# Kernel optimization log

Measured on AMD Instinct MI355X. Metric: run time of the kernel, lower is better.

Reference implementation:

```python
import jax, jax.numpy as jnp
import numpy as np

B = 16        # graphs per batch
NPG = 4096    # nodes per graph
N = B * NPG
EPG = 32768   # edges per graph
E = B * EPG
F_NODE, F_EDGE, G, H, A = 8, 4, 16, 128, 10


def setup_inputs() -> dict:
    key = jax.random.key(0)
    ks = jax.random.split(key, 32)
    x = jax.random.normal(ks[0], (N, F_NODE), jnp.float32)
    # random intra-graph edges, offset into the batched node id space
    src = jax.random.randint(ks[1], (B, EPG), 0, NPG)
    dst = jax.random.randint(ks[2], (B, EPG), 0, NPG)
    off = (jnp.arange(B) * NPG)[:, None]
    edge_index = jnp.stack([(src + off).reshape(-1), (dst + off).reshape(-1)]).astype(jnp.int64)
    edge_attr = jax.random.normal(ks[3], (E, F_EDGE), jnp.float32)
    global_state = jax.random.normal(ks[4], (B, G), jnp.float32)
    current_pipe_nodes = jax.random.randint(ks[5], (B, 2), 0, NPG).astype(jnp.int64)

    def w(k, shape):
        fan_in = shape[0] if len(shape) > 1 else shape[0]
        return jax.random.normal(k, shape, jnp.float32) * (1.0 / np.sqrt(fan_in))

    return dict(
        x=x, edge_index=edge_index, edge_attr=edge_attr,
        global_state=global_state, current_pipe_nodes=current_pipe_nodes,
        W_l1=w(ks[6], (F_NODE, H)), W_r1=w(ks[7], (F_NODE, H)), W_e1=w(ks[8], (F_EDGE, H)),
        att1=w(ks[9], (H,)), b1=jnp.zeros((H,), jnp.float32),
        W_l2=w(ks[10], (H, H)), W_r2=w(ks[11], (H, H)), W_e2=w(ks[12], (F_EDGE, H)),
        att2=w(ks[13], (H,)), b2=jnp.zeros((H,), jnp.float32),
        W_c=w(ks[14], (H + 2 * H + G, 256)), b_c=jnp.zeros((256,), jnp.float32),
        W_a1=w(ks[15], (256, 128)), b_a1=jnp.zeros((128,), jnp.float32),
        W_a2=w(ks[16], (128, A)), b_a2=jnp.zeros((A,), jnp.float32),
        W_v1=w(ks[17], (256, 128)), b_v1=jnp.zeros((128,), jnp.float32),
        W_v2=w(ks[18], (128, 1)), b_v2=jnp.zeros((1,), jnp.float32),
    )


def add_self_loops(edge_index, edge_attr, n):
    # PyG default: add_self_loops=True, fill_value='mean' -> loop attr is the
    # mean of incoming edge_attr per node (zeros if none).
    dst = edge_index[1]
    deg = jax.ops.segment_sum(jnp.ones(dst.shape, jnp.float32), dst, num_segments=n)
    loop_attr = jax.ops.segment_sum(edge_attr, dst, num_segments=n) / jnp.maximum(deg, 1.0)[:, None]
    loops = jnp.tile(jnp.arange(n, dtype=edge_index.dtype)[None, :], (2, 1))
    ei = jnp.concatenate([edge_index, loops], axis=1)
    ea = jnp.concatenate([edge_attr, loop_attr], axis=0)
    return ei, ea


def gatv2(x, ei, ea, Wl, Wr, We, att, bias, n):
    # GATv2Conv (heads=1): score = att . leaky_relu(Wl x_j + Wr x_i + We e_ij)
    # message = alpha_ij * (Wl x_j); segment softmax over incoming edges of i.
    src, dst = ei[0], ei[1]
    xl = x @ Wl                                   # [N,H]
    xr = x @ Wr                                   # [N,H]
    m = xl[src] + xr[dst] + ea @ We               # [E,H]
    s = jax.nn.leaky_relu(m, 0.2) @ att           # [E]
    smax = jax.ops.segment_max(s, dst, num_segments=n)
    ealpha = jnp.exp(s - smax[dst])
    denom = jax.ops.segment_sum(ealpha, dst, num_segments=n)
    alpha = ealpha / denom[dst]
    out = jax.ops.segment_sum(alpha[:, None] * xl[src], dst, num_segments=n)
    return out + bias


def reference(x, edge_index, edge_attr, global_state, current_pipe_nodes,
              W_l1, W_r1, W_e1, att1, b1,
              W_l2, W_r2, W_e2, att2, b2,
              W_c, b_c, W_a1, b_a1, W_a2, b_a2, W_v1, b_v1, W_v2, b_v2):
    ei, ea = add_self_loops(edge_index, edge_attr, N)
    h = jax.nn.relu(gatv2(x, ei, ea, W_l1, W_r1, W_e1, att1, b1, N))
    h = gatv2(h, ei, ea, W_l2, W_r2, W_e2, att2, b2, N)
    # global_mean_pool: graphs are contiguous equal-size blocks
    graph_emb = h.reshape(B, NPG, H).mean(axis=1)                       # [B,H]
    abs_idx = current_pipe_nodes + (jnp.arange(B) * NPG)[:, None]       # [B,2]
    pipe_emb = h[abs_idx.reshape(-1)].reshape(B, 2 * H)                 # [B,2H]
    comb = jnp.concatenate([graph_emb, pipe_emb, global_state], axis=1)
    feat = jax.nn.relu(comb @ W_c + b_c)
    logits = jax.nn.relu(feat @ W_a1 + b_a1) @ W_a2 + b_a2              # [B,A]
    value = jax.nn.relu(feat @ W_v1 + b_v1) @ W_v2 + b_v2               # [B,1]
    return jnp.concatenate([logits, value], axis=1)                     # [B,A+1]
```

## Files before the change

kernel.cpp:

```cpp
#include <hip/hip_runtime.h>
#include <math.h>

#define NN   65536
#define NPG  4096
#define NB   16
#define NE   524288
#define EPG  32768
#define SB   8
#define NH   128
#define FN   8
#define FE   4
#define NG   16
#define NA   10
#define NFRAG 2048
#define L1B  512

typedef __attribute__((ext_vector_type(8))) short bf16x8;
typedef __attribute__((ext_vector_type(4))) float f32x4;

static __device__ __forceinline__ short bf16rne(float f) {
    unsigned u = __builtin_bit_cast(unsigned, f);
    u += 0x7FFFu + ((u >> 16) & 1u);
    return (short)(u >> 16);
}

__global__ __launch_bounds__(1024) void hist_kernel(
        const int* __restrict__ ei, int* __restrict__ subhist,
        const float* __restrict__ Wl2, const float* __restrict__ Wr2,
        bf16x8* __restrict__ wbf) {
    int bid = blockIdx.x;
    int t = threadIdx.x;
    if (bid < NB * SB) {
        __shared__ int hh[NPG];
        int g = bid >> 3, sb = bid & 7;
        for (int i = t; i < NPG; i += 1024) hh[i] = 0;
        __syncthreads();
        const int* dstp = ei + NE + g * EPG + sb * (EPG / SB);
        for (int i = t; i < EPG / SB; i += 1024)
            atomicAdd(&hh[dstp[i] - g * NPG], 1);
        __syncthreads();
        int* out = subhist + (size_t)bid * NPG;
        for (int i = t; i < NPG; i += 1024) out[i] = hh[i];
    } else {
        int sel = bid - NB * SB;
        const float* W = sel ? Wr2 : Wl2;
#pragma unroll
        for (int q = 0; q < 2; ++q) {
            int f = t * 2 + q;
            int lane = f & 63;
            int kgct = f >> 6;
            int kg = kgct & 3, ct = kgct >> 2;
            int kbase = kg * 32 + (lane >> 4) * 8;
            int c = ct * 16 + (lane & 15);
            bf16x8 v;
#pragma unroll
            for (int j = 0; j < 8; ++j)
                v[j] = bf16rne(W[(kbase + j) * NH + c]);
            wbf[sel * NFRAG + f] = v;
        }
    }
}

__global__ __launch_bounds__(1024) void csr_lin1_kernel(
        const int* __restrict__ ei, const int* __restrict__ subhist,
        int* __restrict__ offs, int2* __restrict__ csr,
        const float* __restrict__ x,
        const float* __restrict__ Wl, const float* __restrict__ Wr,
        float* __restrict__ xl, float* __restrict__ xr) {
    int bid = blockIdx.x;
    int t = threadIdx.x;
    if (bid < NB * SB) {
        __shared__ int cur[NPG];
        __shared__ int psum[1024];
        int g = bid >> 3, sb = bid & 7;
        int base4 = t * 4;
        int dpre[4], loc[4];
        int run = 0;
#pragma unroll
        for (int i = 0; i < 4; ++i) {
            int nl = base4 + i;
            int d = 0, pre = 0;
#pragma unroll
            for (int s = 0; s < SB; ++s) {
                int v = subhist[((size_t)(g * SB + s)) * NPG + nl];
                pre += (s < sb) ? v : 0;
                d += v;
            }
            dpre[i] = pre;
            loc[i] = run;
            run += d;
        }
        psum[t] = run;
        __syncthreads();
        for (int s = 1; s < 1024; s <<= 1) {
            int add = (t >= s) ? psum[t - s] : 0;
            __syncthreads();
            psum[t] += add;
            __syncthreads();
        }
        int prefix = (t == 0) ? 0 : psum[t - 1];
        int ebase = g * EPG;
#pragma unroll
        for (int i = 0; i < 4; ++i) {
            int nl = base4 + i;
            int off = ebase + prefix + loc[i];
            cur[nl] = off + dpre[i];
            if (sb == 0) offs[g * NPG + nl] = off;
        }
        if (sb == 0 && g == NB - 1 && t == 0) offs[NN] = NE;
        __syncthreads();
        int e0 = g * EPG + sb * (EPG / SB);
#pragma unroll
        for (int i = 0; i < (EPG / SB) / 1024; ++i) {
            int e = e0 + i * 1024 + t;
            int dst = ei[NE + e];
            int src = ei[e];
            int pos = atomicAdd(&cur[dst - g * NPG], 1);
            csr[pos] = make_int2(src, e);
        }
    } else {
        int lb = bid - NB * SB;
        int k = t & 127;
        int oct = t >> 7;
        float wl[FN], wr[FN];
#pragma unroll
        for (int j = 0; j < FN; ++j) {
            wl[j] = Wl[j * NH + k];
            wr[j] = Wr[j * NH + k];
        }
        int nbase = lb * 128 + oct * 16;
        for (int i = 0; i < 16; ++i) {
            int n = nbase + i;
            float4 xa = *(const float4*)&x[(size_t)n * FN];
            float4 xb = *(const float4*)&x[(size_t)n * FN + 4];
            float al = xa.x * wl[0] + xa.y * wl[1] + xa.z * wl[2] + xa.w * wl[3]
                     + xb.x * wl[4] + xb.y * wl[5] + xb.z * wl[6] + xb.w * wl[7];
            float ar = xa.x * wr[0] + xa.y * wr[1] + xa.z * wr[2] + xa.w * wr[3]
                     + xb.x * wr[4] + xb.y * wr[5] + xb.z * wr[6] + xb.w * wr[7];
            xl[(size_t)n * NH + k] = al;
            xr[(size_t)n * NH + k] = ar;
        }
    }
}

__global__ __launch_bounds__(256) void gat_gather_kernel(
        const float4* __restrict__ xl, const float4* __restrict__ xr,
        const float4* __restrict__ ea,
        const int2* __restrict__ csr, const int* __restrict__ offs,
        const float* __restrict__ We, const float* __restrict__ att,
        const float* __restrict__ bias,
        unsigned short* __restrict__ hbf_out,
        float4* __restrict__ lattr_w, const float4* __restrict__ lattr_r,
        float4* __restrict__ gpart, float4* __restrict__ pipe,
        const int* __restrict__ cpn, int do_relu) {
    __shared__ float4 red[8][32];
    int grp = threadIdx.x >> 5;
    int lane = threadIdx.x & 31;
    int bid = blockIdx.x;
    int xcd = bid & 7, slot = bid >> 3;
    int g = xcd + ((slot >> 9) << 3);
    int blk = slot & 511;
    int node = g * NPG + blk * 8 + grp;

    float4 xr4 = xr[node * 32 + lane];
    float4 att4 = ((const float4*)att)[lane];
    const float4* We4 = (const float4*)We;
    float4 we0 = We4[lane];
    float4 we1 = We4[32 + lane];
    float4 we2 = We4[64 + lane];
    float4 we3 = We4[96 + lane];

    int beg = offs[node], end = offs[node + 1];
    float l = 0.f;
    float4 acc = make_float4(0.f, 0.f, 0.f, 0.f);
    float4 easum = make_float4(0.f, 0.f, 0.f, 0.f);
    bool have_lattr = (lattr_r != nullptr);
    if (beg < end) {
        int last = end - 1;
        int2 se0 = csr[beg];
        int p1 = (beg + 1 <= last) ? beg + 1 : last;
        int2 se1 = csr[p1];
        float4 xl0 = xl[se0.x * 32 + lane];
        float4 a0 = ea[se0.y];
        for (int p = beg; p < end; ++p) {
            int p2 = (p + 2 <= last) ? p + 2 : last;
            int2 se2 = csr[p2];
            float4 xl1 = xl[se1.x * 32 + lane];
            float4 a1 = ea[se1.y];
            if (!have_lattr) {
                easum.x += a0.x; easum.y += a0.y; easum.z += a0.z; easum.w += a0.w;
            }
            float tx = xl0.x + xr4.x + a0.x * we0.x + a0.y * we1.x + a0.z * we2.x + a0.w * we3.x;
            float ty = xl0.y + xr4.y + a0.x * we0.y + a0.y * we1.y + a0.z * we2.y + a0.w * we3.y;
            float tz = xl0.z + xr4.z + a0.x * we0.z + a0.y * we1.z + a0.z * we2.z + a0.w * we3.z;
            float tw = xl0.w + xr4.w + a0.x * we0.w + a0.y * we1.w + a0.z * we2.w + a0.w * we3.w;
            tx = tx > 0.f ? tx : 0.2f * tx;
            ty = ty > 0.f ? ty : 0.2f * ty;
            tz = tz > 0.f ? tz : 0.2f * tz;
            tw = tw > 0.f ? tw : 0.2f * tw;
            float s = tx * att4.x + ty * att4.y + tz * att4.z + tw * att4.w;
#pragma unroll
            for (int o = 16; o >= 1; o >>= 1) s += __shfl_xor(s, o);
            float w = __expf(s);
            l += w;
            acc.x += w * xl0.x;
            acc.y += w * xl0.y;
            acc.z += w * xl0.z;
            acc.w += w * xl0.w;
            se1 = se2; xl0 = xl1; a0 = a1;
        }
    }
    {
        float ax, ay, az, aw;
        if (have_lattr) {
            float4 la = lattr_r[node];
            ax = la.x; ay = la.y; az = la.z; aw = la.w;
        } else {
            int deg = end - beg;
            float invd = 1.0f / (float)(deg > 0 ? deg : 1);
            ax = easum.x * invd; ay = easum.y * invd;
            az = easum.z * invd; aw = easum.w * invd;
            if (lane == 0) lattr_w[node] = make_float4(ax, ay, az, aw);
        }
        float4 xl4 = xl[node * 32 + lane];
        float tx = xl4.x + xr4.x + ax * we0.x + ay * we1.x + az * we2.x + aw * we3.x;
        float ty = xl4.y + xr4.y + ax * we0.y + ay * we1.y + az * we2.y + aw * we3.y;
        float tz = xl4.z + xr4.z + ax * we0.z + ay * we1.z + az * we2.z + aw * we3.z;
        float tw = xl4.w + xr4.w + ax * we0.w + ay * we1.w + az * we2.w + aw * we3.w;
        tx = tx > 0.f ? tx : 0.2f * tx;
        ty = ty > 0.f ? ty : 0.2f * ty;
        tz = tz > 0.f ? tz : 0.2f * tz;
        tw = tw > 0.f ? tw : 0.2f * tw;
        float s = tx * att4.x + ty * att4.y + tz * att4.z + tw * att4.w;
#pragma unroll
        for (int o = 16; o >= 1; o >>= 1) s += __shfl_xor(s, o);
        float w = __expf(s);
        l += w;
        acc.x += w * xl4.x;
        acc.y += w * xl4.y;
        acc.z += w * xl4.z;
        acc.w += w * xl4.w;
    }
    float inv = 1.0f / l;
    float4 b4 = ((const float4*)bias)[lane];
    float4 o4;
    o4.x = acc.x * inv + b4.x;
    o4.y = acc.y * inv + b4.y;
    o4.z = acc.z * inv + b4.z;
    o4.w = acc.w * inv + b4.w;
    if (do_relu) {
        o4.x = fmaxf(o4.x, 0.f); o4.y = fmaxf(o4.y, 0.f);
        o4.z = fmaxf(o4.z, 0.f); o4.w = fmaxf(o4.w, 0.f);
    }
    if (hbf_out != nullptr) {
        int rt = node >> 4, m = node & 15;
        int kg = lane >> 3, qd = (lane & 7) >> 1, j0 = (lane & 1) * 4;
        ushort4 v;
        v.x = (unsigned short)bf16rne(o4.x);
        v.y = (unsigned short)bf16rne(o4.y);
        v.z = (unsigned short)bf16rne(o4.z);
        v.w = (unsigned short)bf16rne(o4.w);
        *(ushort4*)&hbf_out[(size_t)(((rt * 4 + kg) * 64 + qd * 16 + m)) * 8 + j0] = v;
    } else {
        int nl = node - g * NPG;
        if (nl == cpn[g * 2 + 0]) pipe[(g * 2 + 0) * 32 + lane] = o4;
        if (nl == cpn[g * 2 + 1]) pipe[(g * 2 + 1) * 32 + lane] = o4;
    }

    if (gpart != nullptr) {
        red[grp][lane] = o4;
        __syncthreads();
        if (grp < 4) {
            float4 o = red[grp + 4][lane];
            red[grp][lane] = make_float4(red[grp][lane].x + o.x, red[grp][lane].y + o.y,
                                         red[grp][lane].z + o.z, red[grp][lane].w + o.w);
        }
        __syncthreads();
        if (grp < 2) {
            float4 o = red[grp + 2][lane];
            red[grp][lane] = make_float4(red[grp][lane].x + o.x, red[grp][lane].y + o.y,
                                         red[grp][lane].z + o.z, red[grp][lane].w + o.w);
        }
        __syncthreads();
        if (grp == 0) {
            float4 a = red[0][lane], b = red[1][lane];
            gpart[(g * 512 + blk) * 32 + lane] =
                make_float4(a.x + b.x, a.y + b.y, a.z + b.z, a.w + b.w);
        }
    }
}

__global__ __launch_bounds__(256) void lin2_mfma_kernel(
        const bf16x8* __restrict__ hbf, const bf16x8* __restrict__ wbf,
        float* __restrict__ xl, float* __restrict__ xr) {
    const bf16x8* Bf = wbf + (size_t)blockIdx.y * NFRAG;
    float* C = blockIdx.y ? xr : xl;
    int t = threadIdx.x;
    int wv = t >> 6, lane = t & 63;
    int rt = blockIdx.x * 4 + wv;
    int row0 = rt * 16;
    int m = lane & 15, qd = lane >> 4;
    bf16x8 afrag[4];
#pragma unroll
    for (int kg = 0; kg < 4; ++kg)
        afrag[kg] = hbf[(size_t)(rt * 4 + kg) * 64 + lane];
#pragma unroll
    for (int ct = 0; ct < 8; ++ct) {
        f32x4 acc = {0.f, 0.f, 0.f, 0.f};
#pragma unroll
        for (int kg = 0; kg < 4; ++kg) {
            bf16x8 b = Bf[((ct << 2) | kg) * 64 + lane];
            acc = __builtin_amdgcn_mfma_f32_16x16x32_bf16(afrag[kg], b, acc, 0, 0, 0);
        }
        int col = ct * 16 + m;
#pragma unroll
        for (int r = 0; r < 4; ++r)
            C[(size_t)(row0 + qd * 4 + r) * NH + col] = acc[r];
    }
}

__global__ __launch_bounds__(1024) void head_kernel(
        const float* __restrict__ gpart, const float* __restrict__ pipe,
        const float* __restrict__ gstate,
        const float* __restrict__ Wc, const float* __restrict__ bc,
        const float* __restrict__ Wa1, const float* __restrict__ ba1,
        const float* __restrict__ Wa2, const float* __restrict__ ba2,
        const float* __restrict__ Wv1, const float* __restrict__ bv1,
        const float* __restrict__ Wv2, const float* __restrict__ bv2,
        float* __restrict__ out) {
    int b = blockIdx.x, t = threadIdx.x;
    __shared__ float comb[400];
    __shared__ float part[4][256];
    __shared__ float pp[8][128];
    __shared__ float feat[256];
    __shared__ float hid[256];
    {
        int d = t & 127, p = t >> 7;
        const float* gp = gpart + (size_t)b * 512 * NH + d;
        float s = 0.f;
        int c0 = p * 64;
        for (int c = c0; c < c0 + 64; ++c) s += gp[c * NH];
        pp[p][d] = s;
    }
    if (t >= 128 && t < 384) comb[t] = pipe[(size_t)b * 2 * NH + (t - 128)];
    else if (t >= 384 && t < 400) comb[t] = gstate[b * NG + (t - 384)];
    __syncthreads();
    if (t < 128) {
        float s = pp[0][t] + pp[1][t] + pp[2][t] + pp[3][t]
                + pp[4][t] + pp[5][t] + pp[6][t] + pp[7][t];
        comb[t] = s * (1.0f / NPG);
    }
    __syncthreads();
    {
        int col = t & 255, p = t >> 8;
        float a = 0.f;
        int j0 = p * 100;
        for (int j = j0; j < j0 + 100; ++j) a += comb[j] * Wc[j * 256 + col];
        part[p][col] = a;
    }
    __syncthreads();
    if (t < 256)
        feat[t] = fmaxf(bc[t] + part[0][t] + part[1][t] + part[2][t] + part[3][t], 0.f);
    __syncthreads();
    {
        int col = t & 255, p = t >> 8;
        const float* W = (col < 128) ? Wa1 : Wv1;
        int cc = col & 127;
        float a = 0.f;
        int j0 = p * 64;
        for (int j = j0; j < j0 + 64; ++j) a += feat[j] * W[j * 128 + cc];
        part[p][col] = a;
    }
    __syncthreads();
    if (t < 256) {
        float bias = (t < 128) ? ba1[t] : bv1[t - 128];
        hid[t] = fmaxf(bias + part[0][t] + part[1][t] + part[2][t] + part[3][t], 0.f);
    }
    __syncthreads();
    if (t < NA) {
        float a2 = ba2[t];
        for (int j = 0; j < NH; ++j) a2 += hid[j] * Wa2[j * NA + t];
        out[b * 11 + t] = a2;
    } else if (t == NA) {
        float a2 = bv2[0];
        for (int j = 0; j < NH; ++j) a2 += hid[128 + j] * Wv2[j];
        out[b * 11 + 10] = a2;
    }
}

extern "C" void kernel_launch(void* const* d_in, const int* in_sizes, int n_in,
                              void* d_out, int out_size, void* d_ws, size_t ws_size,
                              hipStream_t stream) {
    const float* x      = (const float*)d_in[0];
    const int*   ei     = (const int*)d_in[1];
    const float* ea     = (const float*)d_in[2];
    const float* gstate = (const float*)d_in[3];
    const int*   cpn    = (const int*)d_in[4];
    const float* Wl1 = (const float*)d_in[5];
    const float* Wr1 = (const float*)d_in[6];
    const float* We1 = (const float*)d_in[7];
    const float* att1= (const float*)d_in[8];
    const float* b1  = (const float*)d_in[9];
    const float* Wl2 = (const float*)d_in[10];
    const float* Wr2 = (const float*)d_in[11];
    const float* We2 = (const float*)d_in[12];
    const float* att2= (const float*)d_in[13];
    const float* b2  = (const float*)d_in[14];
    const float* Wc  = (const float*)d_in[15];
    const float* bc  = (const float*)d_in[16];
    const float* Wa1 = (const float*)d_in[17];
    const float* ba1 = (const float*)d_in[18];
    const float* Wa2 = (const float*)d_in[19];
    const float* ba2 = (const float*)d_in[20];
    const float* Wv1 = (const float*)d_in[21];
    const float* bv1 = (const float*)d_in[22];
    const float* Wv2 = (const float*)d_in[23];
    const float* bv2 = (const float*)d_in[24];

    char* ws = (char*)d_ws;
    size_t o = 0;
    float* xl     = (float*)(ws + o); o += (size_t)NN * NH * 4;
    float* xr     = (float*)(ws + o); o += (size_t)NN * NH * 4;
    unsigned short* hbf = (unsigned short*)(ws + o); o += (size_t)NN * NH * 2;
    float* lattr  = (float*)(ws + o); o += (size_t)NN * 16;
    float* gpart  = (float*)(ws + o); o += (size_t)NB * 512 * NH * 4;
    float* pipe   = (float*)(ws + o); o += (size_t)NB * 2 * NH * 4;
    int*   offs   = (int*)(ws + o);   o += (((size_t)(NN + 1) * 4 + 255) & ~(size_t)255);
    int*   subhist= (int*)(ws + o);   o += (size_t)NB * SB * NPG * 4;
    int2*  csr    = (int2*)(ws + o);  o += (size_t)NE * 8;
    bf16x8* wbf   = (bf16x8*)(ws + o); o += (size_t)2 * NFRAG * 16;
    (void)o; (void)ws_size; (void)in_sizes; (void)n_in; (void)out_size;

    hist_kernel<<<NB * SB + 2, 1024, 0, stream>>>(ei, subhist, Wl2, Wr2, wbf);
    csr_lin1_kernel<<<NB * SB + L1B, 1024, 0, stream>>>(ei, subhist, offs, csr,
                                                        x, Wl1, Wr1, xl, xr);
    gat_gather_kernel<<<NN / 8, 256, 0, stream>>>((const float4*)xl, (const float4*)xr,
        (const float4*)ea, csr, offs, We1, att1, b1, hbf,
        (float4*)lattr, nullptr, nullptr, nullptr, cpn, 1);
    lin2_mfma_kernel<<<dim3(NN / 64, 2), 256, 0, stream>>>((const bf16x8*)hbf, wbf, xl, xr);
    gat_gather_kernel<<<NN / 8, 256, 0, stream>>>((const float4*)xl, (const float4*)xr,
        (const float4*)ea, csr, offs, We2, att2, b2, nullptr,
        nullptr, (const float4*)lattr, (float4*)gpart, (float4*)pipe, cpn, 0);
    head_kernel<<<NB, 1024, 0, stream>>>(gpart, pipe, gstate, Wc, bc, Wa1, ba1, Wa2, ba2,
                                         Wv1, bv1, Wv2, bv2, (float*)d_out);
}
```

Measured before the change: 270.2 us.

## Fuse histogram into CSR build by recomputing full per-graph histogram in each block

Result: no change. 271.4 us (+0.4%).

```diff
diff --git a/kernel.cpp b/kernel.cpp
--- a/kernel.cpp
+++ b/kernel.cpp
@@ -24,24 +24,68 @@
     return (short)(u >> 16);
 }
 
-__global__ __launch_bounds__(1024) void hist_kernel(
-        const int* __restrict__ ei, int* __restrict__ subhist,
+__global__ __launch_bounds__(1024) void csr_lin1_kernel(
+        const int* __restrict__ ei,
+        int* __restrict__ offs, int2* __restrict__ csr,
+        const float* __restrict__ x,
+        const float* __restrict__ Wl, const float* __restrict__ Wr,
         const float* __restrict__ Wl2, const float* __restrict__ Wr2,
-        bf16x8* __restrict__ wbf) {
+        bf16x8* __restrict__ wbf,
+        float* __restrict__ xl, float* __restrict__ xr) {
     int bid = blockIdx.x;
     int t = threadIdx.x;
     if (bid < NB * SB) {
-        __shared__ int hh[NPG];
+        __shared__ int htot[NPG];
+        __shared__ int hpre[NPG];
+        __shared__ int psum[1024];
         int g = bid >> 3, sb = bid & 7;
-        for (int i = t; i < NPG; i += 1024) hh[i] = 0;
-        __syncthreads();
-        const int* dstp = ei + NE + g * EPG + sb * (EPG / SB);
-        for (int i = t; i < EPG / SB; i += 1024)
-            atomicAdd(&hh[dstp[i] - g * NPG], 1);
-        __syncthreads();
-        int* out = subhist + (size_t)bid * NPG;
-        for (int i = t; i < NPG; i += 1024) out[i] = hh[i];
-    } else {
+        for (int i = t; i < NPG; i += 1024) { htot[i] = 0; hpre[i] = 0; }
+        __syncthreads();
+        const int* dstp = ei + NE + g * EPG;
+        for (int s = 0; s < SB; ++s) {
+            bool pre = s < sb;
+            const int* dc = dstp + s * (EPG / SB);
+            for (int i = t; i < EPG / SB; i += 1024) {
+                int dl = dc[i] - g * NPG;
+                atomicAdd(&htot[dl], 1);
+                if (pre) atomicAdd(&hpre[dl], 1);
+            }
+        }
+        __syncthreads();
+        int base4 = t * 4;
+        int loc[4];
+        int run = 0;
+#pragma unroll
+        for (int i = 0; i < 4; ++i) { loc[i] = run; run += htot[base4 + i]; }
+        psum[t] = run;
+        __syncthreads();
+        for (int s = 1; s < 1024; s <<= 1) {
+            int add = (t >= s) ? psum[t - s] : 0;
+            __syncthreads();
+            psum[t] += add;
+            __syncthreads();
+        }
+        int prefix = (t == 0) ? 0 : psum[t - 1];
+        int ebase = g * EPG;
+#pragma unroll
+        for (int i = 0; i < 4; ++i) {
+            int nl = base4 + i;
+            int off = ebase + prefix + loc[i];
+            hpre[nl] += off;
+            if (sb == 0) offs[g * NPG + nl] = off;
+        }
+        if (sb == 0 && g == NB - 1 && t == 0) offs[NN] = NE;
+        __syncthreads();
+        int e0 = g * EPG + sb * (EPG / SB);
+#pragma unroll
+        for (int i = 0; i < (EPG / SB) / 1024; ++i) {
+            int e = e0 + i * 1024 + t;
+            int dst = ei[NE + e];
+            int src = ei[e];
+            int pos = atomicAdd(&hpre[dst - g * NPG], 1);
+            csr[pos] = make_int2(src, e);
+        }
+    } else if (bid < NB * SB + 2) {
         int sel = bid - NB * SB;
         const float* W = sel ? Wr2 : Wl2;
 #pragma unroll
@@ -58,68 +102,8 @@
                 v[j] = bf16rne(W[(kbase + j) * NH + c]);
             wbf[sel * NFRAG + f] = v;
         }
-    }
-}
-
-__global__ __launch_bounds__(1024) void csr_lin1_kernel(
-        const int* __restrict__ ei, const int* __restrict__ subhist,
-        int* __restrict__ offs, int2* __restrict__ csr,
-        const float* __restrict__ x,
-        const float* __restrict__ Wl, const float* __restrict__ Wr,
-        float* __restrict__ xl, float* __restrict__ xr) {
-    int bid = blockIdx.x;
-    int t = threadIdx.x;
-    if (bid < NB * SB) {
-        __shared__ int cur[NPG];
-        __shared__ int psum[1024];
-        int g = bid >> 3, sb = bid & 7;
-        int base4 = t * 4;
-        int dpre[4], loc[4];
-        int run = 0;
-#pragma unroll
-        for (int i = 0; i < 4; ++i) {
-            int nl = base4 + i;
-            int d = 0, pre = 0;
-#pragma unroll
-            for (int s = 0; s < SB; ++s) {
-                int v = subhist[((size_t)(g * SB + s)) * NPG + nl];
-                pre += (s < sb) ? v : 0;
-                d += v;
-            }
-            dpre[i] = pre;
-            loc[i] = run;
-            run += d;
-        }
-        psum[t] = run;
-        __syncthreads();
-        for (int s = 1; s < 1024; s <<= 1) {
-            int add = (t >= s) ? psum[t - s] : 0;
-            __syncthreads();
-            psum[t] += add;
-            __syncthreads();
-        }
-        int prefix = (t == 0) ? 0 : psum[t - 1];
-        int ebase = g * EPG;
-#pragma unroll
-        for (int i = 0; i < 4; ++i) {
-            int nl = base4 + i;
-            int off = ebase + prefix + loc[i];
-            cur[nl] = off + dpre[i];
-            if (sb == 0) offs[g * NPG + nl] = off;
-        }
-        if (sb == 0 && g == NB - 1 && t == 0) offs[NN] = NE;
-        __syncthreads();
-        int e0 = g * EPG + sb * (EPG / SB);
-#pragma unroll
-        for (int i = 0; i < (EPG / SB) / 1024; ++i) {
-            int e = e0 + i * 1024 + t;
-            int dst = ei[NE + e];
-            int src = ei[e];
-            int pos = atomicAdd(&cur[dst - g * NPG], 1);
-            csr[pos] = make_int2(src, e);
-        }
     } else {
-        int lb = bid - NB * SB;
+        int lb = bid - NB * SB - 2;
         int k = t & 127;
         int oct = t >> 7;
         float wl[FN], wr[FN];
@@ -426,14 +410,12 @@
     float* gpart  = (float*)(ws + o); o += (size_t)NB * 512 * NH * 4;
     float* pipe   = (float*)(ws + o); o += (size_t)NB * 2 * NH * 4;
     int*   offs   = (int*)(ws + o);   o += (((size_t)(NN + 1) * 4 + 255) & ~(size_t)255);
-    int*   subhist= (int*)(ws + o);   o += (size_t)NB * SB * NPG * 4;
     int2*  csr    = (int2*)(ws + o);  o += (size_t)NE * 8;
     bf16x8* wbf   = (bf16x8*)(ws + o); o += (size_t)2 * NFRAG * 16;
     (void)o; (void)ws_size; (void)in_sizes; (void)n_in; (void)out_size;
 
-    hist_kernel<<<NB * SB + 2, 1024, 0, stream>>>(ei, subhist, Wl2, Wr2, wbf);
-    csr_lin1_kernel<<<NB * SB + L1B, 1024, 0, stream>>>(ei, subhist, offs, csr,
-                                                        x, Wl1, Wr1, xl, xr);
+    csr_lin1_kernel<<<NB * SB + 2 + L1B, 1024, 0, stream>>>(ei, offs, csr,
+        x, Wl1, Wr1, Wl2, Wr2, wbf, xl, xr);
     gat_gather_kernel<<<NN / 8, 256, 0, stream>>>((const float4*)xl, (const float4*)xr,
         (const float4*)ea, csr, offs, We1, att1, b1, hbf,
         (float4*)lattr, nullptr, nullptr, nullptr, cpn, 1);
```
